# Kernel optimization log

Hardware: AMD Instinct MI355X
Metric: run time of the kernel (lower is better)

## Reference

```python
import jax, jax.numpy as jnp
import numpy as np

LN_EPS = 1e-5  # torch nn.LayerNorm default

def _layer_norm(x, g, b):
    mu = x.mean(axis=-1, keepdims=True)
    var = x.var(axis=-1, keepdims=True)
    return (x - mu) / jnp.sqrt(var + LN_EPS) * g + b

def setup_inputs() -> dict:
    key = jax.random.key(0)
    ks = jax.random.split(key, 8)
    B, T, L = 1, 4, 384
    c_z, c_t, H, C = 128, 64, 4, 16
    s = 0.02
    t = jax.random.normal(ks[0], (B, T, L, L, c_t), dtype=jnp.float32)
    z = jax.random.normal(ks[1], (B, L, L, c_z), dtype=jnp.float32)
    template_mask = jax.random.randint(ks[2], (B, T, L), 0, 2).astype(jnp.float32)
    Wq = jax.random.normal(ks[3], (c_z, H * C), dtype=jnp.float32) * s
    Wk = jax.random.normal(ks[4], (c_t, H * C), dtype=jnp.float32) * s
    Wv = jax.random.normal(ks[5], (c_t, H * C), dtype=jnp.float32) * s
    Wo = jax.random.normal(ks[6], (H * C, c_z), dtype=jnp.float32) * s
    bo = jnp.zeros((c_z,), dtype=jnp.float32)
    z_ln_g = jnp.ones((c_z,), dtype=jnp.float32)
    z_ln_b = jnp.zeros((c_z,), dtype=jnp.float32)
    t_ln_g = jnp.ones((c_t,), dtype=jnp.float32)
    t_ln_b = jnp.zeros((c_t,), dtype=jnp.float32)
    return dict(t=t, z=z, template_mask=template_mask,
                z_ln_g=z_ln_g, z_ln_b=z_ln_b, t_ln_g=t_ln_g, t_ln_b=t_ln_b,
                Wq=Wq, Wk=Wk, Wv=Wv, Wo=Wo, bo=bo)

def reference(t, z, template_mask, z_ln_g, z_ln_b, t_ln_g, t_ln_b, Wq, Wk, Wv, Wo, bo):
    B, T, L = t.shape[0], t.shape[1], t.shape[2]
    H, C = 4, 16
    z_norm = _layer_norm(z, z_ln_g, z_ln_b)          # [B,L,L,c_z]
    t_norm = _layer_norm(t, t_ln_g, t_ln_b)          # [B,T,L,L,c_t]
    q = (z_norm @ Wq).reshape(B, L, L, H, C)          # [B,L,L,H,C]
    k = (t_norm @ Wk).reshape(B, T, L, L, H, C)       # [B,T,L,L,H,C]
    v = (t_norm @ Wv).reshape(B, T, L, L, H, C)
    logits = jnp.einsum('bijhc,btijhc->btijh', q, k) / jnp.sqrt(jnp.float32(C))
    # pair_mask[b,t,i,j] = m[b,t,i]*m[b,t,j]
    pair_mask = template_mask[:, :, :, None] * template_mask[:, :, None, :]  # [B,T,L,L]
    logits = jnp.where(pair_mask[..., None] == 0, jnp.float32(-1e9), logits)
    attn = jax.nn.softmax(logits, axis=1)             # softmax over template dim T
    attn = attn * pair_mask[..., None]
    attn = attn / jnp.clip(attn.sum(axis=1, keepdims=True), 1e-8, None)
    out = jnp.einsum('btijh,btijhc->bijhc', attn, v).reshape(B, L, L, H * C)
    return out @ Wo + bo
```

## Files before the change

### kernel.cpp

```cpp
#include <hip/hip_runtime.h>

typedef unsigned int u32;
typedef unsigned short u16;
typedef __attribute__((ext_vector_type(8))) short short8;
typedef __attribute__((ext_vector_type(4))) float f4;

#define MFMA(a, b, c) __builtin_amdgcn_mfma_f32_16x16x32_bf16((a), (b), (c), 0, 0, 0)
#define LL 384
#define NPAIR 147456

__device__ __forceinline__ u16 f2bf(float f) {
    u32 u = __float_as_uint(f);
    u = (u + 0x7fffu + ((u >> 16) & 1u)) >> 16;
    return (u16)u;
}
__device__ __forceinline__ u32 pack2(float a, float b) {
    u32 ua = __float_as_uint(a); ua = (ua + 0x7fffu + ((ua >> 16) & 1u)) >> 16;
    u32 ub = __float_as_uint(b); ub = (ub + 0x7fffu + ((ub >> 16) & 1u)) >> 16;
    return ua | (ub << 16);
}
__device__ __forceinline__ short8 ld8(const u16* p) { return *reinterpret_cast<const short8*>(p); }
__device__ __forceinline__ float red16(float v) {
    v += __shfl_xor(v, 1);
    v += __shfl_xor(v, 2);
    v += __shfl_xor(v, 4);
    v += __shfl_xor(v, 8);
    return v;
}


__global__ void prep_w(const float* __restrict__ Wq, const float* __restrict__ Wk,
                       const float* __restrict__ Wv, const float* __restrict__ Wo,
                       const float* __restrict__ zg, const float* __restrict__ tg,
                       float* __restrict__ ws) {
    int idx = blockIdx.x * blockDim.x + threadIdx.x;
    u16* wsu = (u16*)ws;
    if (idx < 8192) {
        int kb = idx >> 9, rem = idx & 511, n = rem >> 3, j = rem & 7, k = kb * 8 + j;
        wsu[idx] = f2bf(Wq[k * 64 + n] * zg[k]);
    } else if (idx < 12288) {
        int e = idx - 8192;
        int kb = e >> 9, rem = e & 511, n = rem >> 3, j = rem & 7, k = kb * 8 + j;
        wsu[idx] = f2bf(Wk[k * 64 + n] * tg[k]);
    } else if (idx < 16384) {
        int e = idx - 12288;
        int kb = e >> 9, rem = e & 511, n = rem >> 3, j = rem & 7, k = kb * 8 + j;
        wsu[idx] = f2bf(Wv[k * 64 + n] * tg[k]);
    } else if (idx < 24576) {
        int e = idx - 16384;
        int kb = e >> 10, rem = e & 1023, n = rem >> 3, j = rem & 7, k = kb * 8 + j;
        wsu[idx] = f2bf(Wo[k * 128 + n]);
    }
}

__global__ void prep_aux(const float* __restrict__ Wq, const float* __restrict__ Wk,
                         const float* __restrict__ Wv, const float* __restrict__ zg,
                         const float* __restrict__ zb, const float* __restrict__ tg,
                         const float* __restrict__ tb, const float* __restrict__ bo,
                         float* __restrict__ ws) {
    int idx = blockIdx.x * blockDim.x + threadIdx.x;
    if (idx < 384) {
        int g = idx >> 6, hc = idx & 63;
        float acc = 0.f;
        if (g == 0)      { for (int d = 0; d < 128; ++d) acc += zg[d] * Wq[d*64+hc]; ws[12288+hc] = acc; }
        else if (g == 1) { for (int d = 0; d < 128; ++d) acc += zb[d] * Wq[d*64+hc]; ws[12352+hc] = acc; }
        else if (g == 2) { for (int d = 0; d < 64;  ++d) acc += tg[d] * Wk[d*64+hc]; ws[12416+hc] = acc; }
        else if (g == 3) { for (int d = 0; d < 64;  ++d) acc += tb[d] * Wk[d*64+hc]; ws[12480+hc] = acc; }
        else if (g == 4) { for (int d = 0; d < 64;  ++d) acc += tg[d] * Wv[d*64+hc]; ws[12544+hc] = acc; }
        else             { for (int d = 0; d < 64;  ++d) acc += tb[d] * Wv[d*64+hc]; ws[12608+hc] = acc; }
    } else if (idx < 512) {
        ws[12672 + idx - 384] = bo[idx - 384];
    }
}

__global__ __launch_bounds__(256) void tpa_main(
    const float* __restrict__ tmpl,
    const float* __restrict__ z,
    const float* __restrict__ mask,
    const float* __restrict__ ws,
    float* __restrict__ out)
{
    __shared__ __align__(16) u16 sT[4 * 32 * 72];
    __shared__ __align__(16) u16 sZ[32 * 136];
    __shared__ __align__(16) u16 sW[8192];
    __shared__ float sZr[32], sZrm[32];
    __shared__ float sTr[4 * 32], sTrm[4 * 32];
    __shared__ float sAux[384];
    __shared__ float sBo[128];
    __shared__ float sPm[4 * 32];

    const int tid = threadIdx.x;
    const int p0 = blockIdx.x * 32;
    const u16* wsu = (const u16*)ws;

    {
        const uint4* src = (const uint4*)wsu;
        uint4* dst = (uint4*)sW;
        #pragma unroll
        for (int r = 0; r < 4; ++r) dst[tid + 256 * r] = src[tid + 256 * r];
        if (tid < 128) {
            sAux[tid] = ws[12288 + tid];
            sAux[128 + tid] = ws[12416 + tid];
            sAux[256 + tid] = ws[12544 + tid];
            sBo[tid] = ws[12672 + tid];
            int tt = tid >> 5, rr = tid & 31;
            int p = p0 + rr, i = p / LL, j = p - i * LL;
            sPm[tt * 32 + rr] = mask[tt * LL + i] * mask[tt * LL + j];
        }
    }
    {
        int pp = tid >> 3, part = tid & 7;
        const float4* zg4 = (const float4*)(z + (size_t)(p0 + pp) * 128) + part * 4;
        float4 a0 = zg4[0], a1 = zg4[1], a2 = zg4[2], a3 = zg4[3];
        float s = a0.x+a0.y+a0.z+a0.w + a1.x+a1.y+a1.z+a1.w
                + a2.x+a2.y+a2.z+a2.w + a3.x+a3.y+a3.z+a3.w;
        float ss = a0.x*a0.x+a0.y*a0.y+a0.z*a0.z+a0.w*a0.w
                 + a1.x*a1.x+a1.y*a1.y+a1.z*a1.z+a1.w*a1.w
                 + a2.x*a2.x+a2.y*a2.y+a2.z*a2.z+a2.w*a2.w
                 + a3.x*a3.x+a3.y*a3.y+a3.z*a3.z+a3.w*a3.w;
        s += __shfl_xor(s, 1); ss += __shfl_xor(ss, 1);
        s += __shfl_xor(s, 2); ss += __shfl_xor(ss, 2);
        s += __shfl_xor(s, 4); ss += __shfl_xor(ss, 4);
        if (part == 0) {
            float mu = s * (1.f / 128.f);
            float var = fmaf(-mu, mu, ss * (1.f / 128.f));
            float r = rsqrtf(var + 1e-5f);
            sZr[pp] = r; sZrm[pp] = r * mu;
        }
        uint4 w0, w1;
        w0.x = pack2(a0.x, a0.y); w0.y = pack2(a0.z, a0.w);
        w0.z = pack2(a1.x, a1.y); w0.w = pack2(a1.z, a1.w);
        w1.x = pack2(a2.x, a2.y); w1.y = pack2(a2.z, a2.w);
        w1.z = pack2(a3.x, a3.y); w1.w = pack2(a3.z, a3.w);
        uint4* d = (uint4*)(sZ + pp * 136 + part * 16);
        d[0] = w0; d[1] = w1;
    }
    {
        int tt = tid >> 6, pp = (tid >> 1) & 31, part = tid & 1;
        const float4* tg4 = (const float4*)(tmpl + ((size_t)tt * NPAIR + p0 + pp) * 64) + part * 8;
        float s = 0.f, ss = 0.f;
        uint4 wbuf[4];
        #pragma unroll
        for (int c = 0; c < 4; ++c) {
            float4 b0 = tg4[c * 2], b1 = tg4[c * 2 + 1];
            s  += b0.x+b0.y+b0.z+b0.w + b1.x+b1.y+b1.z+b1.w;
            ss += b0.x*b0.x+b0.y*b0.y+b0.z*b0.z+b0.w*b0.w
                + b1.x*b1.x+b1.y*b1.y+b1.z*b1.z+b1.w*b1.w;
            wbuf[c].x = pack2(b0.x, b0.y); wbuf[c].y = pack2(b0.z, b0.w);
            wbuf[c].z = pack2(b1.x, b1.y); wbuf[c].w = pack2(b1.z, b1.w);
        }
        s += __shfl_xor(s, 1); ss += __shfl_xor(ss, 1);
        if (part == 0) {
            float mu = s * (1.f / 64.f);
            float var = fmaf(-mu, mu, ss * (1.f / 64.f));
            float r = rsqrtf(var + 1e-5f);
            sTr[tt * 32 + pp] = r; sTrm[tt * 32 + pp] = r * mu;
        }
        uint4* d = (uint4*)(sT + tt * 2304 + pp * 72 + part * 32);
        d[0] = wbuf[0]; d[1] = wbuf[1]; d[2] = wbuf[2]; d[3] = wbuf[3];
    }
    __syncthreads();

    const int wave = tid >> 6, lane = tid & 63, g = lane >> 4, l15 = lane & 15;
    const int rt = wave & 1, nh = wave >> 1;
    const int rowA = rt * 16 + l15;
    const int h0 = 2 * nh, h1 = 2 * nh + 1;
    const int col0 = h0 * 16 + l15, col1 = h1 * 16 + l15;
    int rowC[4];
    #pragma unroll
    for (int r = 0; r < 4; ++r) rowC[r] = rt * 16 + g * 4 + r;

    f4 aq0 = {0.f,0.f,0.f,0.f}, aq1 = {0.f,0.f,0.f,0.f};
    #pragma unroll
    for (int ks = 0; ks < 4; ++ks) {
        short8 A = ld8(sZ + rowA * 136 + ks * 32 + g * 8);
        int kb = ks * 4 + g;
        short8 B0 = ld8(sW + kb * 512 + col0 * 8);
        short8 B1 = ld8(sW + kb * 512 + col1 * 8);
        aq0 = MFMA(A, B0, aq0);
        aq1 = MFMA(A, B1, aq1);
    }
    float qv[2][4], qg[2][4], qb[2][4];
    {
        float zr_[4], zrm_[4];
        #pragma unroll
        for (int r = 0; r < 4; ++r) { zr_[r] = sZr[rowC[r]]; zrm_[r] = sZrm[rowC[r]]; }
        float GQ0 = sAux[col0], BQ0 = sAux[64 + col0];
        float GQ1 = sAux[col1], BQ1 = sAux[64 + col1];
        #pragma unroll
        for (int r = 0; r < 4; ++r) {
            qv[0][r] = fmaf(zr_[r], aq0[r], fmaf(-zrm_[r], GQ0, BQ0));
            qv[1][r] = fmaf(zr_[r], aq1[r], fmaf(-zrm_[r], GQ1, BQ1));
        }
        float GK0 = sAux[128 + col0], BK0 = sAux[192 + col0];
        float GK1 = sAux[128 + col1], BK1 = sAux[192 + col1];
        #pragma unroll
        for (int r = 0; r < 4; ++r) {
            qg[0][r] = red16(qv[0][r] * GK0);
            qb[0][r] = red16(qv[0][r] * BK0);
            qg[1][r] = red16(qv[1][r] * GK1);
            qb[1][r] = red16(qv[1][r] * BK1);
        }
    }
    __syncthreads();
    {
        const uint4* src = (const uint4*)wsu;
        uint4* dst = (uint4*)sW;
        dst[tid]       = src[1024 + tid];
        dst[256 + tid] = src[1280 + tid];
        dst[512 + tid] = src[1536 + tid];
        dst[768 + tid] = src[1792 + tid];
    }
    __syncthreads();

    float lg[4][2][4], pmr[4][4];
    #pragma unroll
    for (int tt = 0; tt < 4; ++tt) {
        f4 k0 = {0.f,0.f,0.f,0.f}, k1 = {0.f,0.f,0.f,0.f};
        const u16* At = sT + tt * 2304;
        #pragma unroll
        for (int ks = 0; ks < 2; ++ks) {
            short8 A = ld8(At + rowA * 72 + ks * 32 + g * 8);
            int kb = ks * 4 + g;
            short8 B0 = ld8(sW + kb * 512 + col0 * 8);
            short8 B1 = ld8(sW + kb * 512 + col1 * 8);
            k0 = MFMA(A, B0, k0);
            k1 = MFMA(A, B1, k1);
        }
        float tr_[4], trm_[4];
        #pragma unroll
        for (int r = 0; r < 4; ++r) {
            tr_[r] = sTr[tt * 32 + rowC[r]];
            trm_[r] = sTrm[tt * 32 + rowC[r]];
            pmr[tt][r] = sPm[tt * 32 + rowC[r]];
        }
        #pragma unroll
        for (int r = 0; r < 4; ++r) {
            float raw0 = red16(qv[0][r] * k0[r]);
            float raw1 = red16(qv[1][r] * k1[r]);
            float l0 = 0.25f * fmaf(tr_[r], raw0, fmaf(-trm_[r], qg[0][r], qb[0][r]));
            float l1 = 0.25f * fmaf(tr_[r], raw1, fmaf(-trm_[r], qg[1][r], qb[1][r]));
            lg[tt][0][r] = (pmr[tt][r] == 0.f) ? -1e9f : l0;
            lg[tt][1][r] = (pmr[tt][r] == 0.f) ? -1e9f : l1;
        }
    }

    float ap[4][2][4], cb[2][4], cg[2][4];
    #pragma unroll
    for (int r = 0; r < 4; ++r) {
        float trA[4], trmA[4];
        #pragma unroll
        for (int tt = 0; tt < 4; ++tt) {
            trA[tt] = sTr[tt * 32 + rowC[r]];
            trmA[tt] = sTrm[tt * 32 + rowC[r]];
        }
        #pragma unroll
        for (int nn = 0; nn < 2; ++nn) {
            float l0 = lg[0][nn][r], l1 = lg[1][nn][r], l2 = lg[2][nn][r], l3 = lg[3][nn][r];
            float mx = fmaxf(fmaxf(l0, l1), fmaxf(l2, l3));
            float e0 = __expf(l0 - mx), e1 = __expf(l1 - mx), e2 = __expf(l2 - mx), e3 = __expf(l3 - mx);
            float inv = 1.f / (e0 + e1 + e2 + e3);
            float a0 = e0 * inv * pmr[0][r], a1 = e1 * inv * pmr[1][r];
            float a2 = e2 * inv * pmr[2][r], a3 = e3 * inv * pmr[3][r];
            float ssum = a0 + a1 + a2 + a3;
            float rr = 1.f / fmaxf(ssum, 1e-8f);
            a0 *= rr; a1 *= rr; a2 *= rr; a3 *= rr;
            cb[nn][r] = a0 + a1 + a2 + a3;
            cg[nn][r] = a0 * trmA[0] + a1 * trmA[1] + a2 * trmA[2] + a3 * trmA[3];
            ap[0][nn][r] = a0 * trA[0]; ap[1][nn][r] = a1 * trA[1];
            ap[2][nn][r] = a2 * trA[2]; ap[3][nn][r] = a3 * trA[3];
        }
    }

    float o_[2][4] = {{0.f,0.f,0.f,0.f},{0.f,0.f,0.f,0.f}};
    const u16* sWv = sW + 4096;
    #pragma unroll
    for (int tt = 0; tt < 4; ++tt) {
        f4 v0 = {0.f,0.f,0.f,0.f}, v1 = {0.f,0.f,0.f,0.f};
        const u16* At = sT + tt * 2304;
        #pragma unroll
        for (int ks = 0; ks < 2; ++ks) {
            short8 A = ld8(At + rowA * 72 + ks * 32 + g * 8);
            int kb = ks * 4 + g;
            short8 B0 = ld8(sWv + kb * 512 + col0 * 8);
            short8 B1 = ld8(sWv + kb * 512 + col1 * 8);
            v0 = MFMA(A, B0, v0);
            v1 = MFMA(A, B1, v1);
        }
        #pragma unroll
        for (int r = 0; r < 4; ++r) {
            o_[0][r] = fmaf(ap[tt][0][r], v0[r], o_[0][r]);
            o_[1][r] = fmaf(ap[tt][1][r], v1[r], o_[1][r]);
        }
    }
    {
        float GV0 = sAux[256 + col0], BV0 = sAux[320 + col0];
        float GV1 = sAux[256 + col1], BV1 = sAux[320 + col1];
        #pragma unroll
        for (int r = 0; r < 4; ++r) {
            o_[0][r] = fmaf(cb[0][r], BV0, fmaf(-cg[0][r], GV0, o_[0][r]));
            o_[1][r] = fmaf(cb[1][r], BV1, fmaf(-cg[1][r], GV1, o_[1][r]));
        }
    }
    __syncthreads();
    {
        #pragma unroll
        for (int r = 0; r < 4; ++r) {
            sZ[rowC[r] * 72 + col0] = f2bf(o_[0][r]);
            sZ[rowC[r] * 72 + col1] = f2bf(o_[1][r]);
        }
        const uint4* src = (const uint4*)wsu;
        uint4* dst = (uint4*)sW;
        #pragma unroll
        for (int r = 0; r < 4; ++r) dst[tid + 256 * r] = src[2048 + tid + 256 * r];
    }
    __syncthreads();

    {
        const int rt2 = wave & 1;
        const int nb = (wave >> 1) * 4;
        f4 c0 = {0.f,0.f,0.f,0.f}, c1 = {0.f,0.f,0.f,0.f};
        f4 c2 = {0.f,0.f,0.f,0.f}, c3 = {0.f,0.f,0.f,0.f};
        #pragma unroll
        for (int ks = 0; ks < 2; ++ks) {
            short8 A = ld8(sZ + (rt2 * 16 + l15) * 72 + ks * 32 + g * 8);
            int kb = ks * 4 + g;
            short8 B0 = ld8(sW + kb * 1024 + ((nb + 0) * 16 + l15) * 8);
            short8 B1 = ld8(sW + kb * 1024 + ((nb + 1) * 16 + l15) * 8);
            short8 B2 = ld8(sW + kb * 1024 + ((nb + 2) * 16 + l15) * 8);
            short8 B3 = ld8(sW + kb * 1024 + ((nb + 3) * 16 + l15) * 8);
            c0 = MFMA(A, B0, c0); c1 = MFMA(A, B1, c1);
            c2 = MFMA(A, B2, c2); c3 = MFMA(A, B3, c3);
        }
        #pragma unroll
        for (int r = 0; r < 4; ++r) {
            int row = p0 + rt2 * 16 + g * 4 + r;
            float* op = out + (size_t)row * 128;
            op[(nb + 0) * 16 + l15] = c0[r] + sBo[(nb + 0) * 16 + l15];
            op[(nb + 1) * 16 + l15] = c1[r] + sBo[(nb + 1) * 16 + l15];
            op[(nb + 2) * 16 + l15] = c2[r] + sBo[(nb + 2) * 16 + l15];
            op[(nb + 3) * 16 + l15] = c3[r] + sBo[(nb + 3) * 16 + l15];
        }
    }
}

extern "C" void kernel_launch(void* const* d_in, const int* in_sizes, int n_in,
                              void* d_out, int out_size, void* d_ws, size_t ws_size,
                              hipStream_t stream) {
    const float* t   = (const float*)d_in[0];
    const float* z   = (const float*)d_in[1];
    const float* msk = (const float*)d_in[2];
    const float* zg  = (const float*)d_in[3];
    const float* zb  = (const float*)d_in[4];
    const float* tg  = (const float*)d_in[5];
    const float* tb  = (const float*)d_in[6];
    const float* Wq  = (const float*)d_in[7];
    const float* Wk  = (const float*)d_in[8];
    const float* Wv  = (const float*)d_in[9];
    const float* Wo  = (const float*)d_in[10];
    const float* bo  = (const float*)d_in[11];
    float* ws = (float*)d_ws;

    prep_w<<<96, 256, 0, stream>>>(Wq, Wk, Wv, Wo, zg, tg, ws);
    prep_aux<<<2, 256, 0, stream>>>(Wq, Wk, Wv, zg, zb, tg, tb, bo, ws);
    tpa_main<<<4608, 256, 0, stream>>>(t, z, msk, ws, (float*)d_out);
}
```

Baseline: 333.0 us.

## Drop shared weight staging, read weights from global, use DPP reductions

Removes the 16 KB shared-memory weight buffer and its staged copies and syncs, loading bf16 weight fragments straight from the global workspace (expected to be cache-resident) into registers. Shared-memory use falls, and a launch-bounds hint asks for more resident blocks per CU. The 16-lane shuffle reductions become DPP row operations, and the logit path is simplified: K is normalized before the dot product instead of the precomputed qg/qb correction terms, with a fast reciprocal in the softmax. The risk is global or L2 latency on weight loads, plus more register pressure from the occupancy hint.

```diff
diff --git a/kernel.cpp b/kernel.cpp
--- a/kernel.cpp
+++ b/kernel.cpp
@@ -20,11 +20,17 @@
     return ua | (ub << 16);
 }
 __device__ __forceinline__ short8 ld8(const u16* p) { return *reinterpret_cast<const short8*>(p); }
+
+template <int CTRL>
+__device__ __forceinline__ float dpp_add(float v) {
+    int t = __builtin_amdgcn_update_dpp(0, __float_as_int(v), CTRL, 0xf, 0xf, true);
+    return v + __int_as_float(t);
+}
 __device__ __forceinline__ float red16(float v) {
-    v += __shfl_xor(v, 1);
-    v += __shfl_xor(v, 2);
-    v += __shfl_xor(v, 4);
-    v += __shfl_xor(v, 8);
+    v = dpp_add<0xB1>(v);
+    v = dpp_add<0x4E>(v);
+    v = dpp_add<0x124>(v);
+    v = dpp_add<0x128>(v);
     return v;
 }
 
@@ -73,7 +79,7 @@
     }
 }
 
-__global__ __launch_bounds__(256) void tpa_main(
+__global__ __launch_bounds__(256, 5) void tpa_main(
     const float* __restrict__ tmpl,
     const float* __restrict__ z,
     const float* __restrict__ mask,
@@ -82,7 +88,6 @@
 {
     __shared__ __align__(16) u16 sT[4 * 32 * 72];
     __shared__ __align__(16) u16 sZ[32 * 136];
-    __shared__ __align__(16) u16 sW[8192];
     __shared__ float sZr[32], sZrm[32];
     __shared__ float sTr[4 * 32], sTrm[4 * 32];
     __shared__ float sAux[384];
@@ -93,20 +98,14 @@
     const int p0 = blockIdx.x * 32;
     const u16* wsu = (const u16*)ws;
 
-    {
-        const uint4* src = (const uint4*)wsu;
-        uint4* dst = (uint4*)sW;
-        #pragma unroll
-        for (int r = 0; r < 4; ++r) dst[tid + 256 * r] = src[tid + 256 * r];
-        if (tid < 128) {
-            sAux[tid] = ws[12288 + tid];
-            sAux[128 + tid] = ws[12416 + tid];
-            sAux[256 + tid] = ws[12544 + tid];
-            sBo[tid] = ws[12672 + tid];
-            int tt = tid >> 5, rr = tid & 31;
-            int p = p0 + rr, i = p / LL, j = p - i * LL;
-            sPm[tt * 32 + rr] = mask[tt * LL + i] * mask[tt * LL + j];
-        }
+    if (tid < 128) {
+        sAux[tid]       = ws[12288 + tid];
+        sAux[128 + tid] = ws[12416 + tid];
+        sAux[256 + tid] = ws[12544 + tid];
+        sBo[tid]        = ws[12672 + tid];
+        int tt = tid >> 5, rr = tid & 31;
+        int p = p0 + rr, i = p / LL, j = p - i * LL;
+        sPm[tt * 32 + rr] = mask[tt * LL + i] * mask[tt * LL + j];
     }
     {
         int pp = tid >> 3, part = tid & 7;
@@ -164,8 +163,7 @@
     const int wave = tid >> 6, lane = tid & 63, g = lane >> 4, l15 = lane & 15;
     const int rt = wave & 1, nh = wave >> 1;
     const int rowA = rt * 16 + l15;
-    const int h0 = 2 * nh, h1 = 2 * nh + 1;
-    const int col0 = h0 * 16 + l15, col1 = h1 * 16 + l15;
+    const int col0 = (2 * nh) * 16 + l15, col1 = (2 * nh + 1) * 16 + l15;
     int rowC[4];
     #pragma unroll
     for (int r = 0; r < 4; ++r) rowC[r] = rt * 16 + g * 4 + r;
@@ -174,167 +172,134 @@
     #pragma unroll
     for (int ks = 0; ks < 4; ++ks) {
         short8 A = ld8(sZ + rowA * 136 + ks * 32 + g * 8);
-        int kb = ks * 4 + g;
-        short8 B0 = ld8(sW + kb * 512 + col0 * 8);
-        short8 B1 = ld8(sW + kb * 512 + col1 * 8);
-        aq0 = MFMA(A, B0, aq0);
-        aq1 = MFMA(A, B1, aq1);
-    }
-    float qv[2][4], qg[2][4], qb[2][4];
-    {
-        float zr_[4], zrm_[4];
-        #pragma unroll
-        for (int r = 0; r < 4; ++r) { zr_[r] = sZr[rowC[r]]; zrm_[r] = sZrm[rowC[r]]; }
+        const u16* wb = wsu + (ks * 4 + g) * 512;
+        aq0 = MFMA(A, ld8(wb + col0 * 8), aq0);
+        aq1 = MFMA(A, ld8(wb + col1 * 8), aq1);
+    }
+    float qv[2][4];
+    {
         float GQ0 = sAux[col0], BQ0 = sAux[64 + col0];
         float GQ1 = sAux[col1], BQ1 = sAux[64 + col1];
         #pragma unroll
         for (int r = 0; r < 4; ++r) {
-            qv[0][r] = fmaf(zr_[r], aq0[r], fmaf(-zrm_[r], GQ0, BQ0));
-            qv[1][r] = fmaf(zr_[r], aq1[r], fmaf(-zrm_[r], GQ1, BQ1));
-        }
+            float zr = sZr[rowC[r]], zm = sZrm[rowC[r]];
+            qv[0][r] = 0.25f * fmaf(zr, aq0[r], fmaf(-zm, GQ0, BQ0));
+            qv[1][r] = 0.25f * fmaf(zr, aq1[r], fmaf(-zm, GQ1, BQ1));
+        }
+    }
+
+    float lg[4][2][4];
+    {
+        const u16* wk = wsu + 8192;
+        short8 Bk00 = ld8(wk + g * 512 + col0 * 8);
+        short8 Bk01 = ld8(wk + g * 512 + col1 * 8);
+        short8 Bk10 = ld8(wk + (4 + g) * 512 + col0 * 8);
+        short8 Bk11 = ld8(wk + (4 + g) * 512 + col1 * 8);
         float GK0 = sAux[128 + col0], BK0 = sAux[192 + col0];
         float GK1 = sAux[128 + col1], BK1 = sAux[192 + col1];
         #pragma unroll
-        for (int r = 0; r < 4; ++r) {
-            qg[0][r] = red16(qv[0][r] * GK0);
-            qb[0][r] = red16(qv[0][r] * BK0);
-            qg[1][r] = red16(qv[1][r] * GK1);
-            qb[1][r] = red16(qv[1][r] * BK1);
-        }
-    }
-    __syncthreads();
-    {
-        const uint4* src = (const uint4*)wsu;
-        uint4* dst = (uint4*)sW;
-        dst[tid]       = src[1024 + tid];
-        dst[256 + tid] = src[1280 + tid];
-        dst[512 + tid] = src[1536 + tid];
-        dst[768 + tid] = src[1792 + tid];
-    }
-    __syncthreads();
-
-    float lg[4][2][4], pmr[4][4];
-    #pragma unroll
-    for (int tt = 0; tt < 4; ++tt) {
-        f4 k0 = {0.f,0.f,0.f,0.f}, k1 = {0.f,0.f,0.f,0.f};
-        const u16* At = sT + tt * 2304;
-        #pragma unroll
-        for (int ks = 0; ks < 2; ++ks) {
-            short8 A = ld8(At + rowA * 72 + ks * 32 + g * 8);
-            int kb = ks * 4 + g;
-            short8 B0 = ld8(sW + kb * 512 + col0 * 8);
-            short8 B1 = ld8(sW + kb * 512 + col1 * 8);
-            k0 = MFMA(A, B0, k0);
-            k1 = MFMA(A, B1, k1);
-        }
-        float tr_[4], trm_[4];
-        #pragma unroll
-        for (int r = 0; r < 4; ++r) {
-            tr_[r] = sTr[tt * 32 + rowC[r]];
-            trm_[r] = sTrm[tt * 32 + rowC[r]];
-            pmr[tt][r] = sPm[tt * 32 + rowC[r]];
-        }
-        #pragma unroll
-        for (int r = 0; r < 4; ++r) {
-            float raw0 = red16(qv[0][r] * k0[r]);
-            float raw1 = red16(qv[1][r] * k1[r]);
-            float l0 = 0.25f * fmaf(tr_[r], raw0, fmaf(-trm_[r], qg[0][r], qb[0][r]));
-            float l1 = 0.25f * fmaf(tr_[r], raw1, fmaf(-trm_[r], qg[1][r], qb[1][r]));
-            lg[tt][0][r] = (pmr[tt][r] == 0.f) ? -1e9f : l0;
-            lg[tt][1][r] = (pmr[tt][r] == 0.f) ? -1e9f : l1;
+        for (int tt = 0; tt < 4; ++tt) {
+            const u16* At = sT + tt * 2304 + rowA * 72;
+            short8 A0 = ld8(At + g * 8);
+            short8 A1 = ld8(At + 32 + g * 8);
+            f4 k0 = {0.f,0.f,0.f,0.f}, k1 = {0.f,0.f,0.f,0.f};
+            k0 = MFMA(A0, Bk00, k0); k1 = MFMA(A0, Bk01, k1);
+            k0 = MFMA(A1, Bk10, k0); k1 = MFMA(A1, Bk11, k1);
+            #pragma unroll
+            for (int r = 0; r < 4; ++r) {
+                float tr = sTr[tt * 32 + rowC[r]], tm = sTrm[tt * 32 + rowC[r]];
+                float kc0 = fmaf(tr, k0[r], fmaf(-tm, GK0, BK0));
+                float kc1 = fmaf(tr, k1[r], fmaf(-tm, GK1, BK1));
+                lg[tt][0][r] = red16(qv[0][r] * kc0);
+                lg[tt][1][r] = red16(qv[1][r] * kc1);
+            }
         }
     }
 
     float ap[4][2][4], cb[2][4], cg[2][4];
     #pragma unroll
     for (int r = 0; r < 4; ++r) {
-        float trA[4], trmA[4];
+        float trA[4], tmA[4], pmA[4];
         #pragma unroll
         for (int tt = 0; tt < 4; ++tt) {
             trA[tt] = sTr[tt * 32 + rowC[r]];
-            trmA[tt] = sTrm[tt * 32 + rowC[r]];
+            tmA[tt] = sTrm[tt * 32 + rowC[r]];
+            pmA[tt] = sPm[tt * 32 + rowC[r]];
         }
         #pragma unroll
         for (int nn = 0; nn < 2; ++nn) {
             float l0 = lg[0][nn][r], l1 = lg[1][nn][r], l2 = lg[2][nn][r], l3 = lg[3][nn][r];
             float mx = fmaxf(fmaxf(l0, l1), fmaxf(l2, l3));
-            float e0 = __expf(l0 - mx), e1 = __expf(l1 - mx), e2 = __expf(l2 - mx), e3 = __expf(l3 - mx);
-            float inv = 1.f / (e0 + e1 + e2 + e3);
-            float a0 = e0 * inv * pmr[0][r], a1 = e1 * inv * pmr[1][r];
-            float a2 = e2 * inv * pmr[2][r], a3 = e3 * inv * pmr[3][r];
-            float ssum = a0 + a1 + a2 + a3;
-            float rr = 1.f / fmaxf(ssum, 1e-8f);
-            a0 *= rr; a1 *= rr; a2 *= rr; a3 *= rr;
-            cb[nn][r] = a0 + a1 + a2 + a3;
-            cg[nn][r] = a0 * trmA[0] + a1 * trmA[1] + a2 * trmA[2] + a3 * trmA[3];
+            float e0 = __expf(l0 - mx) * pmA[0];
+            float e1 = __expf(l1 - mx) * pmA[1];
+            float e2 = __expf(l2 - mx) * pmA[2];
+            float e3 = __expf(l3 - mx) * pmA[3];
+            float s = (e0 + e1) + (e2 + e3);
+            float rr = __builtin_amdgcn_rcpf(fmaxf(s, 1e-20f));
+            float a0 = e0 * rr, a1 = e1 * rr, a2 = e2 * rr, a3 = e3 * rr;
+            cb[nn][r] = s * rr;
+            cg[nn][r] = a0 * tmA[0] + a1 * tmA[1] + a2 * tmA[2] + a3 * tmA[3];
             ap[0][nn][r] = a0 * trA[0]; ap[1][nn][r] = a1 * trA[1];
             ap[2][nn][r] = a2 * trA[2]; ap[3][nn][r] = a3 * trA[3];
         }
     }
 
-    float o_[2][4] = {{0.f,0.f,0.f,0.f},{0.f,0.f,0.f,0.f}};
-    const u16* sWv = sW + 4096;
-    #pragma unroll
-    for (int tt = 0; tt < 4; ++tt) {
-        f4 v0 = {0.f,0.f,0.f,0.f}, v1 = {0.f,0.f,0.f,0.f};
-        const u16* At = sT + tt * 2304;
-        #pragma unroll
-        for (int ks = 0; ks < 2; ++ks) {
-            short8 A = ld8(At + rowA * 72 + ks * 32 + g * 8);
-            int kb = ks * 4 + g;
-            short8 B0 = ld8(sWv + kb * 512 + col0 * 8);
-            short8 B1 = ld8(sWv + kb * 512 + col1 * 8);
-            v0 = MFMA(A, B0, v0);
-            v1 = MFMA(A, B1, v1);
-        }
-        #pragma unroll
-        for (int r = 0; r < 4; ++r) {
-            o_[0][r] = fmaf(ap[tt][0][r], v0[r], o_[0][r]);
-            o_[1][r] = fmaf(ap[tt][1][r], v1[r], o_[1][r]);
-        }
-    }
-    {
+    float o0[4] = {0.f,0.f,0.f,0.f}, o1[4] = {0.f,0.f,0.f,0.f};
+    {
+        const u16* wv = wsu + 12288;
+        short8 Bv00 = ld8(wv + g * 512 + col0 * 8);
+        short8 Bv01 = ld8(wv + g * 512 + col1 * 8);
+        short8 Bv10 = ld8(wv + (4 + g) * 512 + col0 * 8);
+        short8 Bv11 = ld8(wv + (4 + g) * 512 + col1 * 8);
+        #pragma unroll
+        for (int tt = 0; tt < 4; ++tt) {
+            const u16* At = sT + tt * 2304 + rowA * 72;
+            short8 A0 = ld8(At + g * 8);
+            short8 A1 = ld8(At + 32 + g * 8);
+            f4 v0 = {0.f,0.f,0.f,0.f}, v1 = {0.f,0.f,0.f,0.f};
+            v0 = MFMA(A0, Bv00, v0); v1 = MFMA(A0, Bv01, v1);
+            v0 = MFMA(A1, Bv10, v0); v1 = MFMA(A1, Bv11, v1);
+            #pragma unroll
+            for (int r = 0; r < 4; ++r) {
+                o0[r] = fmaf(ap[tt][0][r], v0[r], o0[r]);
+                o1[r] = fmaf(ap[tt][1][r], v1[r], o1[r]);
+            }
+        }
         float GV0 = sAux[256 + col0], BV0 = sAux[320 + col0];
         float GV1 = sAux[256 + col1], BV1 = sAux[320 + col1];
         #pragma unroll
         for (int r = 0; r < 4; ++r) {
-            o_[0][r] = fmaf(cb[0][r], BV0, fmaf(-cg[0][r], GV0, o_[0][r]));
-            o_[1][r] = fmaf(cb[1][r], BV1, fmaf(-cg[1][r], GV1, o_[1][r]));
+            o0[r] = fmaf(cb[0][r], BV0, fmaf(-cg[0][r], GV0, o0[r]));
+            o1[r] = fmaf(cb[1][r], BV1, fmaf(-cg[1][r], GV1, o1[r]));
         }
     }
     __syncthreads();
     {
         #pragma unroll
         for (int r = 0; r < 4; ++r) {
-            sZ[rowC[r] * 72 + col0] = f2bf(o_[0][r]);
-            sZ[rowC[r] * 72 + col1] = f2bf(o_[1][r]);
-        }
-        const uint4* src = (const uint4*)wsu;
-        uint4* dst = (uint4*)sW;
-        #pragma unroll
-        for (int r = 0; r < 4; ++r) dst[tid + 256 * r] = src[2048 + tid + 256 * r];
+            sZ[rowC[r] * 72 + col0] = f2bf(o0[r]);
+            sZ[rowC[r] * 72 + col1] = f2bf(o1[r]);
+        }
     }
     __syncthreads();
 
     {
-        const int rt2 = wave & 1;
+        const u16* wo = wsu + 16384;
         const int nb = (wave >> 1) * 4;
         f4 c0 = {0.f,0.f,0.f,0.f}, c1 = {0.f,0.f,0.f,0.f};
         f4 c2 = {0.f,0.f,0.f,0.f}, c3 = {0.f,0.f,0.f,0.f};
         #pragma unroll
         for (int ks = 0; ks < 2; ++ks) {
-            short8 A = ld8(sZ + (rt2 * 16 + l15) * 72 + ks * 32 + g * 8);
-            int kb = ks * 4 + g;
-            short8 B0 = ld8(sW + kb * 1024 + ((nb + 0) * 16 + l15) * 8);
-            short8 B1 = ld8(sW + kb * 1024 + ((nb + 1) * 16 + l15) * 8);
-            short8 B2 = ld8(sW + kb * 1024 + ((nb + 2) * 16 + l15) * 8);
-            short8 B3 = ld8(sW + kb * 1024 + ((nb + 3) * 16 + l15) * 8);
-            c0 = MFMA(A, B0, c0); c1 = MFMA(A, B1, c1);
-            c2 = MFMA(A, B2, c2); c3 = MFMA(A, B3, c3);
+            short8 A = ld8(sZ + rowA * 72 + ks * 32 + g * 8);
+            const u16* wb = wo + (ks * 4 + g) * 1024;
+            c0 = MFMA(A, ld8(wb + ((nb + 0) * 16 + l15) * 8), c0);
+            c1 = MFMA(A, ld8(wb + ((nb + 1) * 16 + l15) * 8), c1);
+            c2 = MFMA(A, ld8(wb + ((nb + 2) * 16 + l15) * 8), c2);
+            c3 = MFMA(A, ld8(wb + ((nb + 3) * 16 + l15) * 8), c3);
         }
         #pragma unroll
         for (int r = 0; r < 4; ++r) {
-            int row = p0 + rt2 * 16 + g * 4 + r;
+            int row = p0 + rowC[r];
             float* op = out + (size_t)row * 128;
             op[(nb + 0) * 16 + l15] = c0[r] + sBo[(nb + 0) * 16 + l15];
             op[(nb + 1) * 16 + l15] = c1[r] + sBo[(nb + 1) * 16 + l15];
```

Result: slower. 366.0 us (+9.9%).
